# Kernel optimization log

Hardware: AMD Instinct MI355X
Metric: run time of the kernel (lower is better)

Reference implementation:

```python
import jax, jax.numpy as jnp
import numpy as np

N_NODES = 50000
N_EDGES = 800000
IN_DIM = 100

def setup_inputs() -> dict:
    key = jax.random.key(0)
    ks = jax.random.split(key, 12)
    nf = jax.random.normal(ks[0], (3, IN_DIM), dtype=jnp.float32)
    tid = jax.random.randint(ks[1], (N_NODES,), 0, 4)
    xr = jax.random.normal(ks[2], (N_NODES, IN_DIM), dtype=jnp.float32)
    # nodes of type 0/1/2 get exact prototype rows; type 3 ('edge') gets random rows
    x = jnp.where((tid < 3)[:, None], nf[jnp.clip(tid, 0, 2)], xr)
    edge_index = jax.random.randint(ks[3], (2, N_EDGES), 0, N_NODES, dtype=jnp.int32)
    def w(k, fi, fo):
        return jax.random.normal(k, (fi, fo), dtype=jnp.float32) * (1.0 / np.sqrt(fi))
    return {
        'x': x, 'node_feature': nf, 'edge_index': edge_index,
        'W1': w(ks[4], 100, 512), 'b1': jnp.zeros((512,), jnp.float32),
        'W2': w(ks[5], 512, 256), 'b2': jnp.zeros((256,), jnp.float32),
        'W3': w(ks[6], 256, 128), 'b3': jnp.zeros((128,), jnp.float32),
        'W4': w(ks[7], 128, 200), 'b4': jnp.zeros((200,), jnp.float32),
    }

def _gcn_forward(x, edge_index, W1, b1, W2, b2, W3, b3, W4, b4):
    N = x.shape[0]
    loop = jnp.arange(N, dtype=edge_index.dtype)
    src = jnp.concatenate([edge_index[0], loop])
    dst = jnp.concatenate([edge_index[1], loop])
    deg = jax.ops.segment_sum(jnp.ones_like(src, dtype=x.dtype), dst, num_segments=N)
    dinv = jnp.where(deg > 0, jax.lax.rsqrt(deg), 0.0)
    norm = dinv[src] * dinv[dst]  # symmetric GCN normalization with self-loops
    def gcn(h, W, b):
        h = h @ W
        agg = jax.ops.segment_sum(h[src] * norm[:, None], dst, num_segments=N)
        return agg + b
    out = jax.nn.relu(gcn(x, W1, b1))
    out = jax.nn.relu(gcn(out, W2, b2))
    out = jax.nn.relu(gcn(out, W3, b3))
    out = jax.nn.relu(gcn(out, W4, b4))
    return out

def _cat_mean(x, out, node_feature):
    # Vectorized replacement of the per-node python loop: output slot order is
    # init(nf0)->0, accept(nf2)->1, edge(other)->2, common(nf1)->3, matching the
    # original append order when all groups are nonempty.
    eq = jnp.all(x[:, None, :] == node_feature[None, :, :], axis=-1)  # [N,3]
    group = jnp.where(eq[:, 0], 0, jnp.where(eq[:, 1], 3, jnp.where(eq[:, 2], 1, 2)))
    sums = jax.ops.segment_sum(out, group, num_segments=4)            # [4,D]
    cnt = jax.ops.segment_sum(jnp.ones((x.shape[0],), out.dtype), group, num_segments=4)
    means = jnp.where(cnt[:, None] > 0, sums / jnp.maximum(cnt, 1.0)[:, None], 0.0)
    return means.reshape(1, -1)  # [1, 4*D]

def reference(x, node_feature, edge_index, W1, b1, W2, b2, W3, b3, W4, b4):
    out = _gcn_forward(x, edge_index, W1, b1, W2, b2, W3, b3, W4, b4)
    return _cat_mean(x, out, node_feature)
```

## Files before the change

### kernel.cpp

```cpp
#include <hip/hip_runtime.h>
#include <stdint.h>

typedef __attribute__((ext_vector_type(8))) short bf16x8;
typedef __attribute__((ext_vector_type(4))) float f32x4;

__device__ __forceinline__ float bf2f(ushort h) {
    union { uint u; float f; } v; v.u = ((uint)h) << 16; return v.f;
}
__device__ __forceinline__ ushort f2bf(float f) {
    union { float f; uint u; } v; v.f = f;
    uint u = v.u;
    return (ushort)((u + 0x7fffu + ((u >> 16) & 1u)) >> 16);
}

__device__ __forceinline__ void gll(const ushort* g, ushort* l) {
    __builtin_amdgcn_global_load_lds(
        (const __attribute__((address_space(1))) void*)g,
        (__attribute__((address_space(3))) void*)l, 16, 0, 0);
}


__device__ __forceinline__ void tr2_one(const float* __restrict__ W,
                                        ushort* __restrict__ WTh, ushort* __restrict__ WTl,
                                        int K, int Nc, int KP, int idx) {
    int n = idx / KP, k = idx % KP;
    float w = (n < Nc && k < K) ? W[(size_t)k * Nc + n] : 0.0f;
    ushort hi = f2bf(w);
    ushort lo = f2bf(w - bf2f(hi));
    WTh[idx] = hi;
    WTl[idx] = lo;
}

__global__ void k_init(const uint* __restrict__ xu, const uint* __restrict__ nfu,
                       ushort* __restrict__ xb, int* __restrict__ gid, int NN,
                       const int* __restrict__ dst, int E, int* __restrict__ deg,
                       const float* __restrict__ W1, const float* __restrict__ W2,
                       const float* __restrict__ W3, const float* __restrict__ W4,
                       ushort* __restrict__ WT1h, ushort* __restrict__ WT1l,
                       ushort* __restrict__ WT2h, ushort* __restrict__ WT2l,
                       ushort* __restrict__ WT3h, ushort* __restrict__ WT3l,
                       ushort* __restrict__ WT4h, ushort* __restrict__ WT4l,
                       int PB, int EB) {
    int b = blockIdx.x;
    if (b < PB) {
        int wid = b * 4 + (threadIdx.x >> 6);
        int lane = threadIdx.x & 63;
        if (wid >= NN) return;
        int c0 = lane * 2;
        uint w = 0u;
        int m0 = 1, m1 = 1, m2 = 1;
        if (c0 < 100) {
            uint2 xv = *(const uint2*)&xu[(size_t)wid * 100 + c0];
            uint2 a = *(const uint2*)&nfu[c0];
            uint2 bb = *(const uint2*)&nfu[100 + c0];
            uint2 c = *(const uint2*)&nfu[200 + c0];
            m0 = (xv.x == a.x) & (xv.y == a.y);
            m1 = (xv.x == bb.x) & (xv.y == bb.y);
            m2 = (xv.x == c.x) & (xv.y == c.y);
            w = (uint)f2bf(__uint_as_float(xv.x)) | ((uint)f2bf(__uint_as_float(xv.y)) << 16);
        }
        int e0 = __all(m0), e1 = __all(m1), e2 = __all(m2);
        *(uint*)&xb[(size_t)wid * 128 + c0] = w;
        if (lane == 0) gid[wid] = e0 ? 0 : (e1 ? 3 : (e2 ? 1 : 2));
    } else if (b < PB + EB) {
        int e = (b - PB) * 256 + threadIdx.x;
        if (e < E) atomicAdd(&deg[dst[e]], 1);
    } else {
        int idx = (b - PB - EB) * 256 + threadIdx.x;
        if (idx < 65536) tr2_one(W1, WT1h, WT1l, 100, 512, 128, idx);
        else if (idx < 196608) tr2_one(W2, WT2h, WT2l, 512, 256, 512, idx - 65536);
        else if (idx < 229376) tr2_one(W3, WT3h, WT3l, 256, 128, 256, idx - 196608);
        else if (idx < 262144) tr2_one(W4, WT4h, WT4l, 128, 200, 128, idx - 229376);
    }
}


__global__ void k_scanA(const int* __restrict__ deg, int* __restrict__ offs,
                        int* __restrict__ bsum, float* __restrict__ dinv,
                        const int* __restrict__ gid, int* __restrict__ gcnt, int NN) {
    __shared__ int lds[256];
    __shared__ int cnt4[4];
    int t = threadIdx.x;
    if (t < 4) cnt4[t] = 0;
    int i = blockIdx.x * 256 + t;
    int v = (i < NN) ? deg[i] : 0;
    if (i < NN) dinv[i] = 1.0f / sqrtf((float)(v + 1));
    lds[t] = v;
    __syncthreads();
    if (i < NN) atomicAdd(&cnt4[gid[i]], 1);
    for (int d = 1; d < 256; d <<= 1) {
        int u = (t >= d) ? lds[t - d] : 0;
        __syncthreads();
        lds[t] += u;
        __syncthreads();
    }
    if (i < NN) offs[i] = lds[t] - v;
    if (t == 255) bsum[blockIdx.x] = lds[255];
    __syncthreads();
    if (t < 4 && cnt4[t]) atomicAdd(&gcnt[t], cnt4[t]);
}


__global__ void k_fill(const int* __restrict__ src, const int* __restrict__ dst, int E,
                       const float* __restrict__ dinv, const int* __restrict__ offs,
                       const int* __restrict__ bsum,
                       int* __restrict__ cur, uint2* __restrict__ epk, int NN, int NB,
                       int* __restrict__ goffs) {
    __shared__ int sex[256];
    int t = threadIdx.x;
    int v = (t < NB) ? bsum[t] : 0;
    sex[t] = v;
    __syncthreads();
    for (int d = 1; d < 256; d <<= 1) {
        int u = (t >= d) ? sex[t - d] : 0;
        __syncthreads();
        sex[t] += u;
        __syncthreads();
    }
    int incl = sex[t];
    __syncthreads();
    sex[t] = incl - v;
    __syncthreads();
    int i = blockIdx.x * 256 + t;
    if (i < NN) goffs[i] = offs[i] + sex[i >> 8];
    if (i >= E) return;
    int s = src[i], d = dst[i];
    int p = offs[d] + sex[d >> 8] + atomicAdd(&cur[d], 1);
    epk[p] = make_uint2((uint)s, __float_as_uint(dinv[s] * dinv[d]));
}


__device__ __forceinline__ uint2 ldnt_u2(const uint2* p) {
    union { unsigned long long ll; uint2 v; } r;
    r.ll = __builtin_nontemporal_load((const unsigned long long*)p);
    return r.v;
}

__device__ __forceinline__ void fma2(uint u, float w, float& a0, float& a1) {
    union { uint u; float f; } lo, hi;
    lo.u = u << 16;
    hi.u = u & 0xffff0000u;
    a0 = fmaf(w, lo.f, a0);
    a1 = fmaf(w, hi.f, a1);
}

template <int UN, int LD>
__device__ __forceinline__ void agg_step(const ushort* __restrict__ Hc,
                                         const uint2* __restrict__ epk, int e,
                                         float& a0, float& a1) {
    uint2 q[UN];
#pragma unroll
    for (int i = 0; i < UN; ++i) q[i] = ldnt_u2(epk + e + i);
    uint u[UN];
#pragma unroll
    for (int i = 0; i < UN; ++i) u[i] = *(const uint*)(Hc + (size_t)q[i].x * LD);
#pragma unroll
    for (int i = 0; i < UN; ++i) fma2(u[i], __uint_as_float(q[i].y), a0, a1);
}

template <int LD, bool BR>
__global__ __launch_bounds__(256) void k_aggs(
        const ushort* __restrict__ H, ushort* __restrict__ outb,
        const float* __restrict__ dinv, const int* __restrict__ offs,
        const int* __restrict__ deg, const uint2* __restrict__ epk,
        const float* __restrict__ bias, int NN, int NNpad) {
    int wid = (int)((blockIdx.x * blockDim.x + threadIdx.x) >> 6);
    int lane = threadIdx.x & 63;
    if (wid >= NNpad) return;
    int c0 = lane * 2;
    ushort* op = outb + (size_t)wid * LD + c0;
    if (wid >= NN) {
        __builtin_nontemporal_store(0u, (uint*)op);
        return;
    }
    const ushort* Hc = H + c0;
    float a0 = 0.0f, a1 = 0.0f;
    {
        float di = dinv[wid];
        float sw = di * di;
        uint u = *(const uint*)(Hc + (size_t)wid * LD);
        fma2(u, sw, a0, a1);
    }
    int e = offs[wid];
    int end = e + deg[wid];
    for (; e + 8 <= end; e += 8) agg_step<8, LD>(Hc, epk, e, a0, a1);
    if (e + 4 <= end) { agg_step<4, LD>(Hc, epk, e, a0, a1); e += 4; }
    if (e + 2 <= end) { agg_step<2, LD>(Hc, epk, e, a0, a1); e += 2; }
    if (e < end) agg_step<1, LD>(Hc, epk, e, a0, a1);
    if (BR) {
        a0 = fmaxf(a0 + bias[c0], 0.0f);
        a1 = fmaxf(a1 + bias[c0 + 1], 0.0f);
    }
    uint w = (uint)f2bf(a0) | ((uint)f2bf(a1) << 16);
    __builtin_nontemporal_store(w, (uint*)op);
}


template <bool BR, int OUT>
__global__ __launch_bounds__(256) void k_gemm(
        const ushort* __restrict__ A,
        const ushort* __restrict__ Bh, const ushort* __restrict__ Bl,
        const float* __restrict__ bias,
        ushort* __restrict__ Cb,
        int Nc, int K, int tNb,
        const int* __restrict__ gid, float* __restrict__ gsum, int NN) {
    __shared__ union {
        ushort st[3][128 * 32];
        float epi[64 * 132];
    } sm;
    __shared__ int gcode[64];
    int bm = blockIdx.x / tNb, bn = blockIdx.x % tNb;
    int m0 = bm * 128, n0 = bn * 128;
    int wv = threadIdx.x >> 6, lane = threadIdx.x & 63;
    int l15 = lane & 15, quad = lane >> 4;
    const ushort* gsrc;
    ushort* ldst;
    int ng;
    if (wv == 0)      { gsrc = A  + (size_t)m0 * K;        ldst = sm.st[0];        ng = 4; }
    else if (wv == 1) { gsrc = A  + (size_t)(m0 + 64) * K; ldst = sm.st[0] + 2048; ng = 4; }
    else if (wv == 2) { gsrc = Bh + (size_t)n0 * K;        ldst = sm.st[1];        ng = 8; }
    else              { gsrc = Bl + (size_t)n0 * K;        ldst = sm.st[2];        ng = 8; }
    const ushort* gBase = gsrc + (size_t)(lane >> 2) * K + (lane & 3) * 8;
    int wm = (wv >> 1) * 64, wn = (wv & 1) * 64;
    const ushort* sA_ = sm.st[0];
    const ushort* sBh_ = sm.st[1];
    const ushort* sBl_ = sm.st[2];
    f32x4 acc[4][4] = {};
    for (int k0 = 0; k0 < K; k0 += 32) {
        for (int i = 0; i < ng; ++i)
            gll(gBase + (size_t)(16 * i) * K + k0, ldst + i * 512);
        __syncthreads();
        bf16x8 Af[4], Bfh[4], Bfl[4];
#pragma unroll
        for (int i = 0; i < 4; ++i) {
            int ra = (wm + 16 * i + l15) * 32 + quad * 8;
            int rb = (wn + 16 * i + l15) * 32 + quad * 8;
            Af[i]  = *(const bf16x8*)(sA_ + ra);
            Bfh[i] = *(const bf16x8*)(sBh_ + rb);
            Bfl[i] = *(const bf16x8*)(sBl_ + rb);
        }
#pragma unroll
        for (int mi = 0; mi < 4; ++mi)
#pragma unroll
            for (int ni = 0; ni < 4; ++ni) {
                acc[mi][ni] = __builtin_amdgcn_mfma_f32_16x16x32_bf16(Af[mi], Bfh[ni], acc[mi][ni], 0, 0, 0);
                acc[mi][ni] = __builtin_amdgcn_mfma_f32_16x16x32_bf16(Af[mi], Bfl[ni], acc[mi][ni], 0, 0, 0);
            }
        __syncthreads();
    }
    float bia[4] = {0.f, 0.f, 0.f, 0.f};
    if (BR) {
#pragma unroll
        for (int ni = 0; ni < 4; ++ni) {
            int col = n0 + wn + 16 * ni + l15;
            if (col < Nc) bia[ni] = bias[col];
        }
    }
    float* epi = sm.epi;
    int t = threadIdx.x;
    float s0 = 0.f, s1 = 0.f, s2 = 0.f, s3 = 0.f;
    int colR = t & 127, rg = t >> 7;
    for (int half = 0; half < 2; ++half) {
        if ((wv >> 1) == half) {
#pragma unroll
            for (int mi = 0; mi < 4; ++mi)
#pragma unroll
                for (int r = 0; r < 4; ++r) {
                    int rl = mi * 16 + quad * 4 + r;
#pragma unroll
                    for (int ni = 0; ni < 4; ++ni) {
                        float v = acc[mi][ni][r];
                        if (BR) v = fmaxf(v + bia[ni], 0.0f);
                        epi[rl * 132 + wn + ni * 16 + l15] = v;
                    }
                }
        }
        if (OUT == 2 && t < 64) {
            int grow = m0 + half * 64 + t;
            gcode[t] = (grow < NN) ? gid[grow] : -1;
        }
        __syncthreads();
        if (OUT == 2) {
#pragma unroll 4
            for (int r = 0; r < 32; ++r) {
                int row = rg * 32 + r;
                int g = gcode[row];
                float v = epi[row * 132 + colR];
                s0 += (g == 0) ? v : 0.f;
                s1 += (g == 1) ? v : 0.f;
                s2 += (g == 2) ? v : 0.f;
                s3 += (g == 3) ? v : 0.f;
            }
        } else {
#pragma unroll
            for (int j = 0; j < 16; ++j) {
                int e = (j * 256 + t) * 2;
                int rl = e >> 7, cl = e & 127;
                int grow = m0 + half * 64 + rl;
                int gcol = n0 + cl;
                float v0 = epi[rl * 132 + cl];
                float v1 = epi[rl * 132 + cl + 1];
                *(uint*)&Cb[(size_t)grow * Nc + gcol] = (uint)f2bf(v0) | ((uint)f2bf(v1) << 16);
            }
        }
        __syncthreads();
    }
    if (OUT == 2) {
        if (rg == 1) {
            epi[colR * 4 + 0] = s0; epi[colR * 4 + 1] = s1;
            epi[colR * 4 + 2] = s2; epi[colR * 4 + 3] = s3;
        }
        __syncthreads();
        if (rg == 0) {
            s0 += epi[colR * 4 + 0]; s1 += epi[colR * 4 + 1];
            s2 += epi[colR * 4 + 2]; s3 += epi[colR * 4 + 3];
            int gcol = n0 + colR;
            if (gcol < Nc) {
                atomicAdd(&gsum[0 * Nc + gcol], s0);
                atomicAdd(&gsum[1 * Nc + gcol], s1);
                atomicAdd(&gsum[2 * Nc + gcol], s2);
                atomicAdd(&gsum[3 * Nc + gcol], s3);
            }
        }
    }
}


__global__ void k_final(const float* __restrict__ gsum, const int* __restrict__ gcnt,
                        float* __restrict__ out) {
    int j = blockIdx.x * blockDim.x + threadIdx.x;
    if (j >= 800) return;
    int c = gcnt[j / 200];
    out[j] = (c > 0) ? gsum[j] / (float)c : 0.0f;
}


extern "C" void kernel_launch(void* const* d_in, const int* in_sizes, int n_in,
                              void* d_out, int out_size, void* d_ws, size_t ws_size,
                              hipStream_t stream) {
    const float* x  = (const float*)d_in[0];
    const float* nf = (const float*)d_in[1];
    const int* ei   = (const int*)d_in[2];
    const float* W1 = (const float*)d_in[3];
    const float* b1 = (const float*)d_in[4];
    const float* W2 = (const float*)d_in[5];
    const float* b2 = (const float*)d_in[6];
    const float* W3 = (const float*)d_in[7];
    const float* b3 = (const float*)d_in[8];
    const float* W4 = (const float*)d_in[9];
    const float* b4 = (const float*)d_in[10];
    float* out = (float*)d_out;

    const int NN = in_sizes[0] / 100;
    const int E  = in_sizes[2] / 2;
    const int MPAD = ((NN + 127) / 128) * 128;
    const int NB = (NN + 255) / 256;
    const int PB = (NN + 3) / 4;
    const int EB = (E + 255) / 256;
    const int TB = 1024;
    const int* src = ei;
    const int* dst = ei + E;

    char* p = (char*)d_ws;
    auto alloc = [&](size_t bytes) -> char* {
        char* r = p;
        p += (bytes + 255) & ~(size_t)255;
        return r;
    };
    char* zz = p;
    int*   deg  = (int*)alloc((size_t)NN * 4);
    int*   cur  = (int*)alloc((size_t)NN * 4);
    float* gsum = (float*)alloc(800 * 4);
    int*   gcnt = (int*)alloc(256);
    size_t zz_bytes = (size_t)(p - zz);
    float* dinv = (float*)alloc((size_t)NN * 4);
    int*   offs = (int*)alloc((size_t)NN * 4);
    int*   goffs = (int*)alloc((size_t)NN * 4);
    int*   bsum = (int*)alloc(1024);
    int*   gid  = (int*)alloc((size_t)NN * 4);
    uint2* epk  = (uint2*)alloc((size_t)E * 8);
    ushort* WT1h = (ushort*)alloc((size_t)512 * 128 * 2);
    ushort* WT1l = (ushort*)alloc((size_t)512 * 128 * 2);
    ushort* WT2h = (ushort*)alloc((size_t)256 * 512 * 2);
    ushort* WT2l = (ushort*)alloc((size_t)256 * 512 * 2);
    ushort* WT3h = (ushort*)alloc((size_t)128 * 256 * 2);
    ushort* WT3l = (ushort*)alloc((size_t)128 * 256 * 2);
    ushort* WT4h = (ushort*)alloc((size_t)256 * 128 * 2);
    ushort* WT4l = (ushort*)alloc((size_t)256 * 128 * 2);
    ushort* xb = (ushort*)alloc((size_t)NN * 128 * 2);
    ushort* P1 = (ushort*)alloc((size_t)MPAD * 128 * 2);
    ushort* H1 = (ushort*)alloc((size_t)MPAD * 512 * 2);
    ushort* T2 = (ushort*)alloc((size_t)MPAD * 256 * 2);
    ushort* H2 = (ushort*)alloc((size_t)MPAD * 256 * 2);
    ushort* T3 = (ushort*)alloc((size_t)MPAD * 128 * 2);
    ushort* H3 = (ushort*)alloc((size_t)MPAD * 128 * 2);
    ushort* P4 = (ushort*)alloc((size_t)MPAD * 128 * 2);

    hipMemsetAsync(zz, 0, zz_bytes, stream);

    k_init<<<PB + EB + TB, 256, 0, stream>>>(
        (const uint*)x, (const uint*)nf, xb, gid, NN, dst, E, deg,
        W1, W2, W3, W4, WT1h, WT1l, WT2h, WT2l, WT3h, WT3l, WT4h, WT4l, PB, EB);
    k_scanA<<<NB, 256, 0, stream>>>(deg, offs, bsum, dinv, gid, gcnt, NN);
    k_fill<<<EB, 256, 0, stream>>>(src, dst, E, dinv, offs, bsum, cur, epk, NN, NB, goffs);

    int aggBlocks = MPAD / 4;
    int mB = MPAD / 128;

    k_aggs<128, false><<<aggBlocks, 256, 0, stream>>>(xb, P1, dinv, goffs, deg, epk, nullptr, NN, MPAD);
    k_gemm<true, 1><<<mB * 4, 256, 0, stream>>>(P1, WT1h, WT1l, b1, H1, 512, 128, 4, nullptr, nullptr, 0);
    k_gemm<false, 1><<<mB * 2, 256, 0, stream>>>(H1, WT2h, WT2l, nullptr, T2, 256, 512, 2, nullptr, nullptr, 0);
    k_aggs<256, true><<<aggBlocks, 256, 0, stream>>>(T2, H2, dinv, goffs, deg, epk, b2, NN, MPAD);
    k_aggs<256, true><<<aggBlocks, 256, 0, stream>>>(T2 + 128, H2 + 128, dinv, goffs, deg, epk, b2 + 128, NN, MPAD);
    k_gemm<false, 1><<<mB * 1, 256, 0, stream>>>(H2, WT3h, WT3l, nullptr, T3, 128, 256, 1, nullptr, nullptr, 0);
    k_aggs<128, true><<<aggBlocks, 256, 0, stream>>>(T3, H3, dinv, goffs, deg, epk, b3, NN, MPAD);
    k_aggs<128, false><<<aggBlocks, 256, 0, stream>>>(H3, P4, dinv, goffs, deg, epk, nullptr, NN, MPAD);
    k_gemm<true, 2><<<mB * 2, 256, 0, stream>>>(P4, WT4h, WT4l, b4, nullptr, 200, 128, 2, gid, gsum, NN);

    k_final<<<4, 256, 0, stream>>>(gsum, gcnt, out);
}
```

Baseline: 462.8 us.

## Split init kernel, record atomic slots, widen 256-col aggregation to one pass

The fused init kernel becomes three separate kernels. The degree-counting atomics now save each edge's slot, so the CSR fill no longer needs a second atomic pass over a cursor array. The aggregation kernel is templated on columns per lane, so the 256-wide layer is done in a single pass with 4 columns per lane instead of two 128-column launches. This halves edge-list reads for that layer. The unroll depth also goes to 16 edges, which raises register use and adds a slot array of E ints.

```diff
diff --git a/kernel.cpp b/kernel.cpp
--- a/kernel.cpp
+++ b/kernel.cpp
@@ -17,6 +17,37 @@
     __builtin_amdgcn_global_load_lds(
         (const __attribute__((address_space(1))) void*)g,
         (__attribute__((address_space(3))) void*)l, 16, 0, 0);
+}
+
+
+__global__ void k_prep(const uint* __restrict__ xu, const uint* __restrict__ nfu,
+                       ushort* __restrict__ xb, int* __restrict__ gid, int NN) {
+    int wid = blockIdx.x * 4 + (threadIdx.x >> 6);
+    int lane = threadIdx.x & 63;
+    if (wid >= NN) return;
+    int c0 = lane * 2;
+    uint w = 0u;
+    int m0 = 1, m1 = 1, m2 = 1;
+    if (c0 < 100) {
+        uint2 xv = *(const uint2*)&xu[(size_t)wid * 100 + c0];
+        uint2 a = *(const uint2*)&nfu[c0];
+        uint2 bb = *(const uint2*)&nfu[100 + c0];
+        uint2 c = *(const uint2*)&nfu[200 + c0];
+        m0 = (xv.x == a.x) & (xv.y == a.y);
+        m1 = (xv.x == bb.x) & (xv.y == bb.y);
+        m2 = (xv.x == c.x) & (xv.y == c.y);
+        w = (uint)f2bf(__uint_as_float(xv.x)) | ((uint)f2bf(__uint_as_float(xv.y)) << 16);
+    }
+    int e0 = __all(m0), e1 = __all(m1), e2 = __all(m2);
+    *(uint*)&xb[(size_t)wid * 128 + c0] = w;
+    if (lane == 0) gid[wid] = e0 ? 0 : (e1 ? 3 : (e2 ? 1 : 2));
+}
+
+
+__global__ void k_deg(const int* __restrict__ dst, int E,
+                      int* __restrict__ deg, int* __restrict__ slot) {
+    int e = blockIdx.x * 256 + threadIdx.x;
+    if (e < E) slot[e] = atomicAdd(&deg[dst[e]], 1);
 }
 
 
@@ -31,47 +62,17 @@
     WTl[idx] = lo;
 }
 
-__global__ void k_init(const uint* __restrict__ xu, const uint* __restrict__ nfu,
-                       ushort* __restrict__ xb, int* __restrict__ gid, int NN,
-                       const int* __restrict__ dst, int E, int* __restrict__ deg,
-                       const float* __restrict__ W1, const float* __restrict__ W2,
-                       const float* __restrict__ W3, const float* __restrict__ W4,
-                       ushort* __restrict__ WT1h, ushort* __restrict__ WT1l,
-                       ushort* __restrict__ WT2h, ushort* __restrict__ WT2l,
-                       ushort* __restrict__ WT3h, ushort* __restrict__ WT3l,
-                       ushort* __restrict__ WT4h, ushort* __restrict__ WT4l,
-                       int PB, int EB) {
-    int b = blockIdx.x;
-    if (b < PB) {
-        int wid = b * 4 + (threadIdx.x >> 6);
-        int lane = threadIdx.x & 63;
-        if (wid >= NN) return;
-        int c0 = lane * 2;
-        uint w = 0u;
-        int m0 = 1, m1 = 1, m2 = 1;
-        if (c0 < 100) {
-            uint2 xv = *(const uint2*)&xu[(size_t)wid * 100 + c0];
-            uint2 a = *(const uint2*)&nfu[c0];
-            uint2 bb = *(const uint2*)&nfu[100 + c0];
-            uint2 c = *(const uint2*)&nfu[200 + c0];
-            m0 = (xv.x == a.x) & (xv.y == a.y);
-            m1 = (xv.x == bb.x) & (xv.y == bb.y);
-            m2 = (xv.x == c.x) & (xv.y == c.y);
-            w = (uint)f2bf(__uint_as_float(xv.x)) | ((uint)f2bf(__uint_as_float(xv.y)) << 16);
-        }
-        int e0 = __all(m0), e1 = __all(m1), e2 = __all(m2);
-        *(uint*)&xb[(size_t)wid * 128 + c0] = w;
-        if (lane == 0) gid[wid] = e0 ? 0 : (e1 ? 3 : (e2 ? 1 : 2));
-    } else if (b < PB + EB) {
-        int e = (b - PB) * 256 + threadIdx.x;
-        if (e < E) atomicAdd(&deg[dst[e]], 1);
-    } else {
-        int idx = (b - PB - EB) * 256 + threadIdx.x;
-        if (idx < 65536) tr2_one(W1, WT1h, WT1l, 100, 512, 128, idx);
-        else if (idx < 196608) tr2_one(W2, WT2h, WT2l, 512, 256, 512, idx - 65536);
-        else if (idx < 229376) tr2_one(W3, WT3h, WT3l, 256, 128, 256, idx - 196608);
-        else if (idx < 262144) tr2_one(W4, WT4h, WT4l, 128, 200, 128, idx - 229376);
-    }
+__global__ void k_wsplit(const float* __restrict__ W1, const float* __restrict__ W2,
+                         const float* __restrict__ W3, const float* __restrict__ W4,
+                         ushort* __restrict__ WT1h, ushort* __restrict__ WT1l,
+                         ushort* __restrict__ WT2h, ushort* __restrict__ WT2l,
+                         ushort* __restrict__ WT3h, ushort* __restrict__ WT3l,
+                         ushort* __restrict__ WT4h, ushort* __restrict__ WT4l) {
+    int idx = blockIdx.x * 256 + threadIdx.x;
+    if (idx < 65536) tr2_one(W1, WT1h, WT1l, 100, 512, 128, idx);
+    else if (idx < 196608) tr2_one(W2, WT2h, WT2l, 512, 256, 512, idx - 65536);
+    else if (idx < 229376) tr2_one(W3, WT3h, WT3l, 256, 128, 256, idx - 196608);
+    else if (idx < 262144) tr2_one(W4, WT4h, WT4l, 128, 200, 128, idx - 229376);
 }
 
 
@@ -101,10 +102,11 @@
 }
 
 
-__global__ void k_fill(const int* __restrict__ src, const int* __restrict__ dst, int E,
+__global__ void k_fill(const int* __restrict__ src, const int* __restrict__ dst,
+                       const int* __restrict__ slot, int E,
                        const float* __restrict__ dinv, const int* __restrict__ offs,
                        const int* __restrict__ bsum,
-                       int* __restrict__ cur, uint2* __restrict__ epk, int NN, int NB,
+                       uint2* __restrict__ epk, int NN, int NB,
                        int* __restrict__ goffs) {
     __shared__ int sex[256];
     int t = threadIdx.x;
@@ -125,7 +127,7 @@
     if (i < NN) goffs[i] = offs[i] + sex[i >> 8];
     if (i >= E) return;
     int s = src[i], d = dst[i];
-    int p = offs[d] + sex[d >> 8] + atomicAdd(&cur[d], 1);
+    int p = offs[d] + sex[d >> 8] + slot[i];
     epk[p] = make_uint2((uint)s, __float_as_uint(dinv[s] * dinv[d]));
 }
 
@@ -144,55 +146,83 @@
     a1 = fmaf(w, hi.f, a1);
 }
 
-template <int UN, int LD>
+template <int CPL>
+__device__ __forceinline__ void ldu(const ushort* p, uint* u) {
+    if constexpr (CPL == 2) {
+        u[0] = *(const uint*)p;
+    } else {
+        uint2 t = *(const uint2*)p;
+        u[0] = t.x; u[1] = t.y;
+    }
+}
+
+template <int UN, int LD, int CPL>
 __device__ __forceinline__ void agg_step(const ushort* __restrict__ Hc,
                                          const uint2* __restrict__ epk, int e,
-                                         float& a0, float& a1) {
+                                         float* a) {
     uint2 q[UN];
 #pragma unroll
     for (int i = 0; i < UN; ++i) q[i] = ldnt_u2(epk + e + i);
-    uint u[UN];
-#pragma unroll
-    for (int i = 0; i < UN; ++i) u[i] = *(const uint*)(Hc + (size_t)q[i].x * LD);
-#pragma unroll
-    for (int i = 0; i < UN; ++i) fma2(u[i], __uint_as_float(q[i].y), a0, a1);
-}
-
-template <int LD, bool BR>
+    uint u[UN][CPL / 2];
+#pragma unroll
+    for (int i = 0; i < UN; ++i) ldu<CPL>(Hc + (size_t)q[i].x * LD, u[i]);
+#pragma unroll
+    for (int i = 0; i < UN; ++i) {
+        float w = __uint_as_float(q[i].y);
+#pragma unroll
+        for (int j = 0; j < CPL / 2; ++j) fma2(u[i][j], w, a[2 * j], a[2 * j + 1]);
+    }
+}
+
+template <int LD, int W, bool BR>
 __global__ __launch_bounds__(256) void k_aggs(
         const ushort* __restrict__ H, ushort* __restrict__ outb,
         const float* __restrict__ dinv, const int* __restrict__ offs,
         const int* __restrict__ deg, const uint2* __restrict__ epk,
         const float* __restrict__ bias, int NN, int NNpad) {
+    constexpr int CPL = W / 64;
     int wid = (int)((blockIdx.x * blockDim.x + threadIdx.x) >> 6);
     int lane = threadIdx.x & 63;
     if (wid >= NNpad) return;
-    int c0 = lane * 2;
+    int c0 = lane * CPL;
     ushort* op = outb + (size_t)wid * LD + c0;
     if (wid >= NN) {
-        __builtin_nontemporal_store(0u, (uint*)op);
+        if constexpr (CPL == 2) __builtin_nontemporal_store(0u, (uint*)op);
+        else __builtin_nontemporal_store(0ull, (unsigned long long*)op);
         return;
     }
     const ushort* Hc = H + c0;
-    float a0 = 0.0f, a1 = 0.0f;
+    float a[CPL];
+#pragma unroll
+    for (int j = 0; j < CPL; ++j) a[j] = 0.0f;
     {
         float di = dinv[wid];
         float sw = di * di;
-        uint u = *(const uint*)(Hc + (size_t)wid * LD);
-        fma2(u, sw, a0, a1);
+        uint u[CPL / 2];
+        ldu<CPL>(Hc + (size_t)wid * LD, u);
+#pragma unroll
+        for (int j = 0; j < CPL / 2; ++j) fma2(u[j], sw, a[2 * j], a[2 * j + 1]);
     }
     int e = offs[wid];
     int end = e + deg[wid];
-    for (; e + 8 <= end; e += 8) agg_step<8, LD>(Hc, epk, e, a0, a1);
-    if (e + 4 <= end) { agg_step<4, LD>(Hc, epk, e, a0, a1); e += 4; }
-    if (e + 2 <= end) { agg_step<2, LD>(Hc, epk, e, a0, a1); e += 2; }
-    if (e < end) agg_step<1, LD>(Hc, epk, e, a0, a1);
+    for (; e + 16 <= end; e += 16) agg_step<16, LD, CPL>(Hc, epk, e, a);
+    if (e + 8 <= end) { agg_step<8, LD, CPL>(Hc, epk, e, a); e += 8; }
+    if (e + 4 <= end) { agg_step<4, LD, CPL>(Hc, epk, e, a); e += 4; }
+    if (e + 2 <= end) { agg_step<2, LD, CPL>(Hc, epk, e, a); e += 2; }
+    if (e < end) agg_step<1, LD, CPL>(Hc, epk, e, a);
     if (BR) {
-        a0 = fmaxf(a0 + bias[c0], 0.0f);
-        a1 = fmaxf(a1 + bias[c0 + 1], 0.0f);
-    }
-    uint w = (uint)f2bf(a0) | ((uint)f2bf(a1) << 16);
-    __builtin_nontemporal_store(w, (uint*)op);
+#pragma unroll
+        for (int j = 0; j < CPL; ++j) a[j] = fmaxf(a[j] + bias[c0 + j], 0.0f);
+    }
+    if constexpr (CPL == 2) {
+        uint w = (uint)f2bf(a[0]) | ((uint)f2bf(a[1]) << 16);
+        __builtin_nontemporal_store(w, (uint*)op);
+    } else {
+        union { uint2 v; unsigned long long ll; } cv;
+        cv.v.x = (uint)f2bf(a[0]) | ((uint)f2bf(a[1]) << 16);
+        cv.v.y = (uint)f2bf(a[2]) | ((uint)f2bf(a[3]) << 16);
+        __builtin_nontemporal_store(cv.ll, (unsigned long long*)op);
+    }
 }
 
 
@@ -369,10 +399,10 @@
     };
     char* zz = p;
     int*   deg  = (int*)alloc((size_t)NN * 4);
-    int*   cur  = (int*)alloc((size_t)NN * 4);
     float* gsum = (float*)alloc(800 * 4);
     int*   gcnt = (int*)alloc(256);
     size_t zz_bytes = (size_t)(p - zz);
+    int*   slot = (int*)alloc((size_t)E * 4);
     float* dinv = (float*)alloc((size_t)NN * 4);
     int*   offs = (int*)alloc((size_t)NN * 4);
     int*   goffs = (int*)alloc((size_t)NN * 4);
@@ -398,23 +428,23 @@
 
     hipMemsetAsync(zz, 0, zz_bytes, stream);
 
-    k_init<<<PB + EB + TB, 256, 0, stream>>>(
-        (const uint*)x, (const uint*)nf, xb, gid, NN, dst, E, deg,
-        W1, W2, W3, W4, WT1h, WT1l, WT2h, WT2l, WT3h, WT3l, WT4h, WT4l, PB, EB);
+    k_prep<<<PB, 256, 0, stream>>>((const uint*)x, (const uint*)nf, xb, gid, NN);
+    k_deg<<<EB, 256, 0, stream>>>(dst, E, deg, slot);
+    k_wsplit<<<TB, 256, 0, stream>>>(W1, W2, W3, W4,
+        WT1h, WT1l, WT2h, WT2l, WT3h, WT3l, WT4h, WT4l);
     k_scanA<<<NB, 256, 0, stream>>>(deg, offs, bsum, dinv, gid, gcnt, NN);
-    k_fill<<<EB, 256, 0, stream>>>(src, dst, E, dinv, offs, bsum, cur, epk, NN, NB, goffs);
+    k_fill<<<EB, 256, 0, stream>>>(src, dst, slot, E, dinv, offs, bsum, epk, NN, NB, goffs);
 
     int aggBlocks = MPAD / 4;
     int mB = MPAD / 128;
 
-    k_aggs<128, false><<<aggBlocks, 256, 0, stream>>>(xb, P1, dinv, goffs, deg, epk, nullptr, NN, MPAD);
+    k_aggs<128, 128, false><<<aggBlocks, 256, 0, stream>>>(xb, P1, dinv, goffs, deg, epk, nullptr, NN, MPAD);
     k_gemm<true, 1><<<mB * 4, 256, 0, stream>>>(P1, WT1h, WT1l, b1, H1, 512, 128, 4, nullptr, nullptr, 0);
     k_gemm<false, 1><<<mB * 2, 256, 0, stream>>>(H1, WT2h, WT2l, nullptr, T2, 256, 512, 2, nullptr, nullptr, 0);
-    k_aggs<256, true><<<aggBlocks, 256, 0, stream>>>(T2, H2, dinv, goffs, deg, epk, b2, NN, MPAD);
-    k_aggs<256, true><<<aggBlocks, 256, 0, stream>>>(T2 + 128, H2 + 128, dinv, goffs, deg, epk, b2 + 128, NN, MPAD);
+    k_aggs<256, 256, true><<<aggBlocks, 256, 0, stream>>>(T2, H2, dinv, goffs, deg, epk, b2, NN, MPAD);
     k_gemm<false, 1><<<mB * 1, 256, 0, stream>>>(H2, WT3h, WT3l, nullptr, T3, 128, 256, 1, nullptr, nullptr, 0);
-    k_aggs<128, true><<<aggBlocks, 256, 0, stream>>>(T3, H3, dinv, goffs, deg, epk, b3, NN, MPAD);
-    k_aggs<128, false><<<aggBlocks, 256, 0, stream>>>(H3, P4, dinv, goffs, deg, epk, nullptr, NN, MPAD);
+    k_aggs<128, 128, true><<<aggBlocks, 256, 0, stream>>>(T3, H3, dinv, goffs, deg, epk, b3, NN, MPAD);
+    k_aggs<128, 128, false><<<aggBlocks, 256, 0, stream>>>(H3, P4, dinv, goffs, deg, epk, nullptr, NN, MPAD);
     k_gemm<true, 2><<<mB * 2, 256, 0, stream>>>(P4, WT4h, WT4l, b4, nullptr, 200, 128, 2, gid, gsum, NN);
 
     k_final<<<4, 256, 0, stream>>>(gsum, gcnt, out);
```

Result: faster. 439.6 us (-5.0%).
